# Performance work log

Hardware: AMD Instinct MI355X
Metric: run time of the kernel (lower is better)

## Reference

```python
import jax, jax.numpy as jnp
import numpy as np

OBS_DIM = 4096
NUM_ACTIONS = 18
ACTION_DIM = 64
D_MODEL = 512
N_LAYERS = 4
HIST = 256
BATCH = 32
D_STATE = 16
D_CONV = 4
EXPAND = 2
D_INNER = EXPAND * D_MODEL           # 1024
DT_RANK = -(-D_MODEL // 16)          # ceil(512/16)=32
OBS_OUT = D_MODEL - ACTION_DIM       # 448


def setup_inputs() -> dict:
    key = jax.random.key(0)
    ks = jax.random.split(key, 16)
    s = 0.02
    inp = {
        "obss": jax.random.normal(ks[0], (BATCH, HIST, OBS_DIM), jnp.float32),
        "actions": jax.random.randint(ks[1], (BATCH, HIST, 1), 0, NUM_ACTIONS),
        "obs_W": jax.random.normal(ks[2], (OBS_OUT, OBS_DIM), jnp.float32) * s,
        "obs_b": jnp.zeros((OBS_OUT,), jnp.float32),
        "act_emb": jax.random.normal(ks[3], (NUM_ACTIONS, ACTION_DIM), jnp.float32) * s,
        "pos_emb": jax.random.normal(ks[4], (1, HIST, D_MODEL), jnp.float32) * s,
        # stacked Mamba params, leading dim = N_LAYERS
        "W_in": jax.random.normal(ks[5], (N_LAYERS, 2 * D_INNER, D_MODEL), jnp.float32) * s,
        "conv_w": jax.random.normal(ks[6], (N_LAYERS, D_INNER, D_CONV), jnp.float32) * s,
        "conv_b": jnp.zeros((N_LAYERS, D_INNER), jnp.float32),
        "W_x": jax.random.normal(ks[7], (N_LAYERS, DT_RANK + 2 * D_STATE, D_INNER), jnp.float32) * s,
        "W_dt": jax.random.normal(ks[8], (N_LAYERS, D_INNER, DT_RANK), jnp.float32) * s,
        "b_dt": jnp.full((N_LAYERS, D_INNER), -4.6, jnp.float32),  # softplus(-4.6)~0.01
        "A_log": jnp.log(jnp.broadcast_to(jnp.arange(1, D_STATE + 1, dtype=jnp.float32), (N_LAYERS, D_INNER, D_STATE))),
        "D_p": jnp.ones((N_LAYERS, D_INNER), jnp.float32),
        "W_out": jax.random.normal(ks[9], (N_LAYERS, D_MODEL, D_INNER), jnp.float32) * s,
        "ffn_W1": jax.random.normal(ks[10], (D_MODEL, D_MODEL), jnp.float32) * s,
        "ffn_b1": jnp.zeros((D_MODEL,), jnp.float32),
        "ffn_W2": jax.random.normal(ks[11], (NUM_ACTIONS, D_MODEL), jnp.float32) * s,
        "ffn_b2": jnp.zeros((NUM_ACTIONS,), jnp.float32),
    }
    return inp


def mamba_block(x, W_in, conv_w, conv_b, W_x, W_dt, b_dt, A_log, D_p, W_out):
    # x: (B, L, D_MODEL)
    B_, L, _ = x.shape
    xz = jnp.einsum('bld,ed->ble', x, W_in)            # (B,L,2*Di)
    xi, z = jnp.split(xz, 2, axis=-1)
    # causal depthwise conv1d, kernel D_CONV
    xp = jnp.pad(xi, ((0, 0), (D_CONV - 1, 0), (0, 0)))
    xc = conv_b + sum(conv_w[:, k] * xp[:, k:k + L, :] for k in range(D_CONV))
    xc = jax.nn.silu(xc)                               # (B,L,Di)
    xdbl = jnp.einsum('bld,ed->ble', xc, W_x)          # (B,L,dt_rank+2*ds)
    dt, Bm, Cm = jnp.split(xdbl, [DT_RANK, DT_RANK + D_STATE], axis=-1)
    dt = jax.nn.softplus(jnp.einsum('blr,dr->bld', dt, W_dt) + b_dt)  # (B,L,Di)
    A = -jnp.exp(A_log)                                # (Di,ds)

    def step(h, inp):
        dt_t, B_t, C_t, x_t = inp                      # (B,Di),(B,ds),(B,ds),(B,Di)
        dA = jnp.exp(dt_t[:, :, None] * A)             # (B,Di,ds)
        h = dA * h + dt_t[:, :, None] * B_t[:, None, :] * x_t[:, :, None]
        y = jnp.einsum('bdn,bn->bd', h, C_t)
        return h, y

    h0 = jnp.zeros((B_, D_INNER, D_STATE), xc.dtype)
    xs = (dt.transpose(1, 0, 2), Bm.transpose(1, 0, 2),
          Cm.transpose(1, 0, 2), xc.transpose(1, 0, 2))
    _, ys = jax.lax.scan(step, h0, xs)                 # (L,B,Di)
    y = ys.transpose(1, 0, 2) + xc * D_p
    y = y * jax.nn.silu(z)
    return jnp.einsum('bld,ed->ble', y, W_out)         # (B,L,D_MODEL)


def reference(obss, actions, obs_W, obs_b, act_emb, pos_emb, W_in, conv_w, conv_b,
              W_x, W_dt, b_dt, A_log, D_p, W_out, ffn_W1, ffn_b1, ffn_W2, ffn_b2):
    L = obss.shape[1]
    tok = jnp.einsum('blo,eo->ble', obss, obs_W) + obs_b          # (B,L,448)
    ae = act_emb[actions[:, :, 0]]                                # (B,L,64)
    # torch.roll(ae, 1, 1) with first step zeroed (history_len > 1)
    ae = jnp.concatenate([jnp.zeros_like(ae[:, :1]), ae[:, :-1]], axis=1)
    x = jnp.concatenate([ae, tok], axis=-1) + pos_emb[:, :L, :]   # (B,L,512)
    for i in range(N_LAYERS):
        x = mamba_block(x, W_in[i], conv_w[i], conv_b[i], W_x[i], W_dt[i],
                        b_dt[i], A_log[i], D_p[i], W_out[i])
    h = jax.nn.relu(jnp.einsum('bld,ed->ble', x, ffn_W1) + ffn_b1)
    out = jnp.einsum('bld,ed->ble', h, ffn_W2) + ffn_b2           # (B,L,18)
    return out[:, -L:, :]
```

## Files before the change

kernel.cpp:

```cpp
#include <hip/hip_runtime.h>
#include <hip/hip_bf16.h>
#include <cstdint>
#include <cstddef>

#define HIST    256
#define DMODEL  512
#define DINNER  1024
#define DSTATE  16
#define DTRANK  32
#define OBSDIM  4096
#define OBSOUT  448
#define ADIM    64
#define NLAYERS 4
#define MROWS   8192

typedef __bf16  bf16x8 __attribute__((ext_vector_type(8)));
typedef float   f32x4  __attribute__((ext_vector_type(4)));

enum { MEPI_TOK = 0, MEPI_BF16 = 1, MEPI_SPLIT = 2, MEPI_RELUB = 3 };

__device__ __forceinline__ float siluf(float x) { return x / (1.f + __expf(-x)); }
__device__ __forceinline__ float softplusf(float x) {
    return fmaxf(x, 0.f) + log1pf(__expf(-fabsf(x)));
}
__device__ __forceinline__ float bflo(unsigned u) { return __uint_as_float(u << 16); }
__device__ __forceinline__ float bfhi(unsigned u) { return __uint_as_float(u & 0xffff0000u); }

template<int EPI>
__global__ __launch_bounds__(256)
void gemm_mfma(const __hip_bfloat16* __restrict__ A, int lda,
               const __hip_bfloat16* __restrict__ W,
               float* __restrict__ Cf, int ldc,
               __hip_bfloat16* __restrict__ Cb, int ldcb,
               int coff, int N, int K, int nbn,
               const float* __restrict__ bias, const float* __restrict__ pos)
{
    __shared__ __hip_bfloat16 Asm[2][128 * 32];
    __shared__ __hip_bfloat16 Bsm[2][128 * 32];
    const int bid = blockIdx.x;
    const int xcd = bid & 7;
    const int s   = bid >> 3;
    const int n_blk = s % nbn;
    const int m_blk = xcd * ((int)(gridDim.x >> 3) / nbn) + s / nbn;
    const int m0 = m_blk * 128;
    const int n0 = n_blk * 128;

    const int tid  = threadIdx.x;
    const int lane = tid & 63;
    const int wv   = tid >> 6;
    const int wm   = (wv >> 1) << 6;
    const int wn   = (wv & 1) << 6;
    const int sr   = lane >> 2;
    const int sc   = (lane & 3) << 3;
    const int quad = lane >> 4;
    const int c16  = lane & 15;

    f32x4 acc[4][4] = {};
    const __hip_bfloat16* aptr = A + (size_t)(m0 + wv * 16 + sr) * lda + sc;
    const __hip_bfloat16* bptr = W + (size_t)(n0 + wv * 16 + sr) * K + sc;

#define STAGE(K0, BUF) { \
    __hip_bfloat16* asml = Asm[BUF] + wv * 16 * 32; \
    __hip_bfloat16* bsml = Bsm[BUF] + wv * 16 * 32; \
    __builtin_amdgcn_global_load_lds( \
        (const __attribute__((address_space(1))) void*)(aptr + (K0)), \
        (__attribute__((address_space(3))) void*)(asml), 16, 0, 0); \
    __builtin_amdgcn_global_load_lds( \
        (const __attribute__((address_space(1))) void*)(aptr + (size_t)64 * lda + (K0)), \
        (__attribute__((address_space(3))) void*)(asml + 64 * 32), 16, 0, 0); \
    __builtin_amdgcn_global_load_lds( \
        (const __attribute__((address_space(1))) void*)(bptr + (K0)), \
        (__attribute__((address_space(3))) void*)(bsml), 16, 0, 0); \
    __builtin_amdgcn_global_load_lds( \
        (const __attribute__((address_space(1))) void*)(bptr + (size_t)64 * K + (K0)), \
        (__attribute__((address_space(3))) void*)(bsml + 64 * 32), 16, 0, 0); \
    }

    STAGE(0, 0)
    __syncthreads();
    int cur = 0;
    for (int k0 = 0; k0 < K; k0 += 32) {
        if (k0 + 32 < K) STAGE(k0 + 32, cur ^ 1)

        bf16x8 af[4], bfr[4];
        #pragma unroll
        for (int i = 0; i < 4; ++i) {
            af[i]  = *(const bf16x8*)(Asm[cur] + (wm + i * 16 + c16) * 32 + quad * 8);
            bfr[i] = *(const bf16x8*)(Bsm[cur] + (wn + i * 16 + c16) * 32 + quad * 8);
        }
        #pragma unroll
        for (int i = 0; i < 4; ++i)
            #pragma unroll
            for (int j = 0; j < 4; ++j)
                acc[i][j] = __builtin_amdgcn_mfma_f32_16x16x32_bf16(af[i], bfr[j], acc[i][j], 0, 0, 0);

        __syncthreads();
        cur ^= 1;
    }
#undef STAGE

    #pragma unroll
    for (int i = 0; i < 4; ++i) {
        const int mbase = m0 + wm + i * 16 + quad * 4;
        #pragma unroll
        for (int j = 0; j < 4; ++j) {
            const int n = n0 + wn + j * 16 + c16;
            if (n < N) {
                #pragma unroll
                for (int r = 0; r < 4; ++r) {
                    const size_t m = mbase + r;
                    float v = acc[i][j][r];
                    if (EPI == MEPI_TOK) {
                        v += bias[n] + pos[(m & (HIST - 1)) * DMODEL + coff + n];
                        Cb[m * ldcb + coff + n] = __float2bfloat16(v);
                    } else if (EPI == MEPI_BF16) {
                        Cb[m * ldcb + n] = __float2bfloat16(v);
                    } else if (EPI == MEPI_SPLIT) {
                        if (n < DTRANK) Cf[m * 32 + n] = v;
                        else Cb[(m >> 1) * 64 + (n & 15) * 4 + (m & 1) * 2 + ((n >> 4) & 1)]
                                 = __float2bfloat16(v);
                    } else {
                        Cb[m * ldcb + n] = __float2bfloat16(fmaxf(v + bias[n], 0.f));
                    }
                }
            }
        }
    }
}

__global__ __launch_bounds__(256)
void gemm_f32_sp(const float* __restrict__ A, int lda,
                 const float* __restrict__ W,
                 __hip_bfloat16* __restrict__ C, int ldc,
                 int N, int K, const float* __restrict__ bias)
{
    __shared__ float As[32][68];
    __shared__ float Ws[32][68];
    const int tid = threadIdx.x;
    const int tx = tid & 15, ty = tid >> 4;
    const int m0 = blockIdx.y * 64;
    const int n0 = blockIdx.x * 64;
    const int lr = tid >> 3;
    const int lc = (tid & 7) << 2;
    float acc[4][4] = {};
    for (int k0 = 0; k0 < K; k0 += 32) {
        const float4 a0 = *(const float4*)(A + (size_t)(m0 + lr) * lda + k0 + lc);
        const float4 a1 = *(const float4*)(A + (size_t)(m0 + lr + 32) * lda + k0 + lc);
        const float4 b0 = *(const float4*)(W + (size_t)(n0 + lr) * K + k0 + lc);
        const float4 b1 = *(const float4*)(W + (size_t)(n0 + lr + 32) * K + k0 + lc);
        __syncthreads();
        As[lc+0][lr] = a0.x; As[lc+1][lr] = a0.y; As[lc+2][lr] = a0.z; As[lc+3][lr] = a0.w;
        As[lc+0][lr+32] = a1.x; As[lc+1][lr+32] = a1.y; As[lc+2][lr+32] = a1.z; As[lc+3][lr+32] = a1.w;
        Ws[lc+0][lr] = b0.x; Ws[lc+1][lr] = b0.y; Ws[lc+2][lr] = b0.z; Ws[lc+3][lr] = b0.w;
        Ws[lc+0][lr+32] = b1.x; Ws[lc+1][lr+32] = b1.y; Ws[lc+2][lr+32] = b1.z; Ws[lc+3][lr+32] = b1.w;
        __syncthreads();
        #pragma unroll
        for (int k = 0; k < 32; ++k) {
            const float4 a4 = *(const float4*)&As[k][ty << 2];
            const float4 b4 = *(const float4*)&Ws[k][tx << 2];
            const float a[4] = {a4.x, a4.y, a4.z, a4.w};
            const float b[4] = {b4.x, b4.y, b4.z, b4.w};
            #pragma unroll
            for (int i = 0; i < 4; ++i)
                #pragma unroll
                for (int j = 0; j < 4; ++j)
                    acc[i][j] = fmaf(a[i], b[j], acc[i][j]);
        }
    }
    const int mb = m0 + (ty << 2);
    const int nb = n0 + (tx << 2);
    #pragma unroll
    for (int i = 0; i < 4; ++i) {
        const size_t m = mb + i;
        #pragma unroll
        for (int j = 0; j < 4; ++j) {
            const int n = nb + j;
            C[m * ldc + n] = __float2bfloat16(softplusf(acc[i][j] + bias[n]));
        }
    }
}

__global__ __launch_bounds__(256)
void cast_bf16_kernel(const float* __restrict__ src, __hip_bfloat16* __restrict__ dst, int n4)
{
    const int i = blockIdx.x * 256 + threadIdx.x;
    if (i >= n4) return;
    const float4 v = ((const float4*)src)[i];
    union { __hip_bfloat16 h[4]; short4 s; } o;
    o.h[0] = __float2bfloat16(v.x); o.h[1] = __float2bfloat16(v.y);
    o.h[2] = __float2bfloat16(v.z); o.h[3] = __float2bfloat16(v.w);
    ((short4*)dst)[i] = o.s;
}

__global__ __launch_bounds__(256)
void cast_pad_kernel(const float* __restrict__ src, __hip_bfloat16* __restrict__ dst,
                     int nrows, int K4, int total4)
{
    const int i = blockIdx.x * 256 + threadIdx.x;
    if (i >= total4) return;
    const int row = i / K4;
    float4 v = make_float4(0.f, 0.f, 0.f, 0.f);
    if (row < nrows) v = ((const float4*)src)[i];
    union { __hip_bfloat16 h[4]; short4 s; } o;
    o.h[0] = __float2bfloat16(v.x); o.h[1] = __float2bfloat16(v.y);
    o.h[2] = __float2bfloat16(v.z); o.h[3] = __float2bfloat16(v.w);
    ((short4*)dst)[i] = o.s;
}

__global__ __launch_bounds__(256)
void embed_kernel(const int* __restrict__ actions, const float* __restrict__ act_emb,
                  const float* __restrict__ pos_emb, __hip_bfloat16* __restrict__ xb)
{
    const int idx = blockIdx.x * 256 + threadIdx.x;
    const int e = idx & 63;
    const int m = idx >> 6;
    const int l = m & (HIST - 1);
    const int b = m >> 8;
    float v = pos_emb[l * DMODEL + e];
    if (l > 0) {
        const int a = actions[b * HIST + l - 1];
        v += act_emb[a * ADIM + e];
    }
    xb[(size_t)m * DMODEL + e] = __float2bfloat16(v);
}

__global__ __launch_bounds__(256)
void conv_silu_kernel(const __hip_bfloat16* __restrict__ xzb, const float* __restrict__ cw,
                      const float* __restrict__ cb, __hip_bfloat16* __restrict__ xcb)
{
    const int idx = blockIdx.x * 256 + threadIdx.x;
    const int d = idx & (DINNER - 1);
    const int m = idx >> 10;
    const int l = m & (HIST - 1);
    const float4 w = ((const float4*)cw)[d];
    const __hip_bfloat16* basep = xzb + (size_t)m * (2 * DINNER) + d;
    float acc = cb[d] + w.w * __bfloat162float(basep[0]);
    if (l >= 1) acc = fmaf(w.z, __bfloat162float(basep[-2 * DINNER]), acc);
    if (l >= 2) acc = fmaf(w.y, __bfloat162float(basep[-4 * DINNER]), acc);
    if (l >= 3) acc = fmaf(w.x, __bfloat162float(basep[-6 * DINNER]), acc);
    xcb[idx] = __float2bfloat16(siluf(acc));
}

__device__ __forceinline__ float dpp_add(float x, const int ctrl) {
    switch (ctrl) {
    case 0xB1:  return x + __int_as_float(__builtin_amdgcn_update_dpp(0, __float_as_int(x), 0xB1, 0xF, 0xF, true));
    case 0x4E:  return x + __int_as_float(__builtin_amdgcn_update_dpp(0, __float_as_int(x), 0x4E, 0xF, 0xF, true));
    case 0x141: return x + __int_as_float(__builtin_amdgcn_update_dpp(0, __float_as_int(x), 0x141, 0xF, 0xF, true));
    default:    return x + __int_as_float(__builtin_amdgcn_update_dpp(0, __float_as_int(x), 0x140, 0xF, 0xF, true));
    }
}

__global__ __launch_bounds__(256)
void scan_kernel(const __hip_bfloat16* __restrict__ dtb, const __hip_bfloat16* __restrict__ bcb,
                 const __hip_bfloat16* __restrict__ xcb, const __hip_bfloat16* __restrict__ zb,
                 const float* __restrict__ A_log, const float* __restrict__ D_p,
                 __hip_bfloat16* __restrict__ yb)
{
    __shared__ unsigned sdx2[128][32];
    __shared__ unsigned sbc2[128][32];
    __shared__ unsigned short sz[256][16];
    const int tid = threadIdx.x;
    const int n   = tid & 15;
    const int g   = tid >> 4;
    const int c0  = blockIdx.x * 16;
    const int b   = c0 >> 10;
    const int d0  = c0 & (DINNER - 1);
    const int d   = d0 + g;
    const size_t row0 = (size_t)b * HIST;

    {
        const uint4* src = (const uint4*)((const unsigned short*)bcb + row0 * 32);
        uint4* dst = (uint4*)&sbc2[0][0];
        #pragma unroll
        for (int i = 0; i < 4; ++i) dst[tid + i * 256] = src[tid + i * 256];
    }
    {
        const int P = tid >> 1, half = tid & 1;
        const size_t m0r = row0 + 2 * P, m1r = m0r + 1;
        const unsigned short* dtu = (const unsigned short*)dtb;
        const unsigned short* xcu = (const unsigned short*)xcb;
        union { uint4 u; unsigned short s[8]; } D0, D1, X0, X1;
        D0.u = *(const uint4*)(dtu + m0r * DINNER + d0 + half * 8);
        D1.u = *(const uint4*)(dtu + m1r * DINNER + d0 + half * 8);
        X0.u = *(const uint4*)(xcu + m0r * DINNER + d0 + half * 8);
        X1.u = *(const uint4*)(xcu + m1r * DINNER + d0 + half * 8);
        #pragma unroll
        for (int gp = 0; gp < 8; ++gp) {
            sdx2[P][(half * 8 + gp) * 2]     = (unsigned)D0.s[gp] | ((unsigned)X0.s[gp] << 16);
            sdx2[P][(half * 8 + gp) * 2 + 1] = (unsigned)D1.s[gp] | ((unsigned)X1.s[gp] << 16);
        }
    }
    {
        const int l = tid >> 1, half = tid & 1;
        const unsigned short* zu = (const unsigned short*)zb;
        #pragma unroll
        for (int i = 0; i < 2; ++i) {
            const int ll = l + i * 128;
            *(uint4*)&sz[ll][half * 8] =
                *(const uint4*)(zu + (row0 + ll) * 2 * DINNER + d0 + half * 8);
        }
    }
    __syncthreads();

    const float A  = -__expf(A_log[d * DSTATE + n]);
    const float Dp = D_p[d];
    float h = 0.f;

    for (int l0 = 0; l0 < HIST; l0 += 16) {
        float yreg = 0.f;
        #pragma unroll
        for (int jp = 0; jp < 8; ++jp) {
            const int P = (l0 >> 1) + jp;
            const uint2 q  = *(const uint2*)&sdx2[P][g * 2];
            const uint2 r2 = *(const uint2*)&sbc2[P][n * 2];
            {
                const float dt = bflo(q.x), xc = bfhi(q.x);
                const float Bv = bflo(r2.x), Cv = bfhi(r2.x);
                const float dA = __expf(dt * A);
                h = fmaf(dA, h, dt * xc * Bv);
                float ctr = h * Cv;
                ctr = dpp_add(ctr, 0xB1);
                ctr = dpp_add(ctr, 0x4E);
                ctr = dpp_add(ctr, 0x141);
                ctr = dpp_add(ctr, 0x140);
                if (n == 2 * jp) yreg = ctr;
            }
            {
                const float dt = bflo(q.y), xc = bfhi(q.y);
                const float Bv = bflo(r2.y), Cv = bfhi(r2.y);
                const float dA = __expf(dt * A);
                h = fmaf(dA, h, dt * xc * Bv);
                float ctr = h * Cv;
                ctr = dpp_add(ctr, 0xB1);
                ctr = dpp_add(ctr, 0x4E);
                ctr = dpp_add(ctr, 0x141);
                ctr = dpp_add(ctr, 0x140);
                if (n == 2 * jp + 1) yreg = ctr;
            }
        }
        const int lr = l0 + n;
        const unsigned short xcu16 =
            ((const unsigned short*)sdx2)[(lr >> 1) * 64 + g * 4 + 1 + 2 * (lr & 1)];
        const float xcf = __uint_as_float(((unsigned)xcu16) << 16);
        const float ze = __uint_as_float(((unsigned)sz[lr][g]) << 16);
        yb[(row0 + lr) * DINNER + d] =
            __float2bfloat16((yreg + xcf * Dp) * siluf(ze));
    }
}

__global__ __launch_bounds__(256)
void ffn2_kernel(const __hip_bfloat16* __restrict__ h, const float* __restrict__ W2,
                 const float* __restrict__ b2, float* __restrict__ out)
{
    const int idx = blockIdx.x * 256 + threadIdx.x;
    const int n = idx & 31;
    const int m = idx >> 5;
    if (n >= 18) return;
    const unsigned short* hr = (const unsigned short*)(h + (size_t)m * DMODEL);
    const float* wr = W2 + (size_t)n * DMODEL;
    float acc = b2[n];
    for (int k = 0; k < DMODEL; k += 8) {
        const uint4 hv = *(const uint4*)(hr + k);
        const float4 w0 = *(const float4*)(wr + k);
        const float4 w1 = *(const float4*)(wr + k + 4);
        acc = fmaf(bflo(hv.x), w0.x, acc);
        acc = fmaf(bfhi(hv.x), w0.y, acc);
        acc = fmaf(bflo(hv.y), w0.z, acc);
        acc = fmaf(bfhi(hv.y), w0.w, acc);
        acc = fmaf(bflo(hv.z), w1.x, acc);
        acc = fmaf(bfhi(hv.z), w1.y, acc);
        acc = fmaf(bflo(hv.w), w1.z, acc);
        acc = fmaf(bfhi(hv.w), w1.w, acc);
    }
    out[(size_t)m * 18 + n] = acc;
}

extern "C" void kernel_launch(void* const* d_in, const int* in_sizes, int n_in,
                              void* d_out, int out_size, void* d_ws, size_t ws_size,
                              hipStream_t stream)
{
    const float* obss    = (const float*)d_in[0];
    const int*   actions = (const int*)  d_in[1];
    const float* obs_W   = (const float*)d_in[2];
    const float* obs_b   = (const float*)d_in[3];
    const float* act_emb = (const float*)d_in[4];
    const float* pos_emb = (const float*)d_in[5];
    const float* W_in    = (const float*)d_in[6];
    const float* conv_w  = (const float*)d_in[7];
    const float* conv_b  = (const float*)d_in[8];
    const float* W_x     = (const float*)d_in[9];
    const float* W_dt    = (const float*)d_in[10];
    const float* b_dt    = (const float*)d_in[11];
    const float* A_log   = (const float*)d_in[12];
    const float* D_p     = (const float*)d_in[13];
    const float* W_out   = (const float*)d_in[14];
    const float* ffn_W1  = (const float*)d_in[15];
    const float* ffn_b1  = (const float*)d_in[16];
    const float* ffn_W2  = (const float*)d_in[17];
    const float* ffn_b2  = (const float*)d_in[18];
    float* out = (float*)d_out;

    const size_t MiB = 1024 * 1024;
    char* base = (char*)d_ws;
    __hip_bfloat16* xb    = (__hip_bfloat16*)(base);
    __hip_bfloat16* xzb   = (__hip_bfloat16*)(base + 8 * MiB);
    __hip_bfloat16* xcb   = (__hip_bfloat16*)(base + 40 * MiB);
    __hip_bfloat16* dtb   = (__hip_bfloat16*)(base + 56 * MiB);
    __hip_bfloat16* yb    = (__hip_bfloat16*)(base + 88 * MiB);
    float*          xdt   = (float*)(base + 104 * MiB);
    __hip_bfloat16* bcb   = (__hip_bfloat16*)(base + 105 * MiB);
    __hip_bfloat16* wbuf  = (__hip_bfloat16*)(base + 106 * MiB);
    __hip_bfloat16* wxb   = (__hip_bfloat16*)(base + 110 * MiB);
    __hip_bfloat16* obssb = (__hip_bfloat16*)(base + 8 * MiB);
    __hip_bfloat16* hbuf  = (__hip_bfloat16*)(base + 8 * MiB);

    cast_bf16_kernel<<<(MROWS * OBSDIM / 4) / 256, 256, 0, stream>>>(obss, obssb, MROWS * OBSDIM / 4);
    cast_pad_kernel<<<(512 * OBSDIM / 4) / 256, 256, 0, stream>>>(obs_W, wbuf, OBSOUT, OBSDIM / 4, 512 * OBSDIM / 4);
    embed_kernel<<<MROWS * ADIM / 256, 256, 0, stream>>>(actions, act_emb, pos_emb, xb);
    gemm_mfma<MEPI_TOK><<<4 * (MROWS / 128), 256, 0, stream>>>(
        obssb, OBSDIM, wbuf, nullptr, 0, xb, DMODEL, ADIM, OBSOUT, OBSDIM, 4, obs_b, pos_emb);

    for (int i = 0; i < NLAYERS; ++i) {
        cast_bf16_kernel<<<(2 * DINNER * DMODEL / 4) / 256, 256, 0, stream>>>(
            W_in + (size_t)i * 2 * DINNER * DMODEL, wbuf, 2 * DINNER * DMODEL / 4);
        gemm_mfma<MEPI_BF16><<<(2 * DINNER / 128) * (MROWS / 128), 256, 0, stream>>>(
            xb, DMODEL, wbuf, nullptr, 0, xzb, 2 * DINNER, 0, 2 * DINNER, DMODEL,
            2 * DINNER / 128, nullptr, nullptr);
        conv_silu_kernel<<<MROWS * DINNER / 256, 256, 0, stream>>>(
            xzb, conv_w + (size_t)i * DINNER * 4, conv_b + (size_t)i * DINNER, xcb);
        cast_pad_kernel<<<(128 * DINNER / 4) / 256, 256, 0, stream>>>(
            W_x + (size_t)i * 64 * DINNER, wxb, 64, DINNER / 4, 128 * DINNER / 4);
        gemm_mfma<MEPI_SPLIT><<<MROWS / 128, 256, 0, stream>>>(
            xcb, DINNER, wxb, xdt, 0, bcb, 0, 0, 64, DINNER, 1, nullptr, nullptr);
        gemm_f32_sp<<<dim3(DINNER / 64, MROWS / 64), 256, 0, stream>>>(
            xdt, 32, W_dt + (size_t)i * DINNER * DTRANK, dtb, DINNER, DINNER, DTRANK,
            b_dt + (size_t)i * DINNER);
        scan_kernel<<<(32 * DINNER) / 16, 256, 0, stream>>>(
            dtb, bcb, xcb, xzb + DINNER, A_log + (size_t)i * DINNER * DSTATE,
            D_p + (size_t)i * DINNER, yb);
        cast_bf16_kernel<<<(DMODEL * DINNER / 4) / 256, 256, 0, stream>>>(
            W_out + (size_t)i * DMODEL * DINNER, wbuf, DMODEL * DINNER / 4);
        gemm_mfma<MEPI_BF16><<<(DMODEL / 128) * (MROWS / 128), 256, 0, stream>>>(
            yb, DINNER, wbuf, nullptr, 0, xb, DMODEL, 0, DMODEL, DINNER,
            DMODEL / 128, nullptr, nullptr);
    }

    cast_bf16_kernel<<<(DMODEL * DMODEL / 4) / 256, 256, 0, stream>>>(ffn_W1, wbuf, DMODEL * DMODEL / 4);
    gemm_mfma<MEPI_RELUB><<<(DMODEL / 128) * (MROWS / 128), 256, 0, stream>>>(
        xb, DMODEL, wbuf, nullptr, 0, hbuf, DMODEL, 0, DMODEL, DMODEL,
        DMODEL / 128, ffn_b1, nullptr);
    ffn2_kernel<<<MROWS * 32 / 256, 256, 0, stream>>>(hbuf, ffn_W2, ffn_b2, out);
}
```

Before: 1.283 ms.

## Double-buffer selective-scan inputs in chunks and overlap loads with recurrence

The scan kernel no longer stages the whole 256-step sequence into shared memory before computing. It now loads 64-step chunks into double-buffered, padded, transposed LDS tiles, prefetching the next chunk into registers while the current one is processed. It also remaps block indices so neighbouring blocks interleave across batches, uses exp2 with a prescaled A, and reads z straight into registers. The intent is to hide global load latency behind the serial recurrence and to cut LDS footprint so more blocks fit per CU, at the cost of more barriers and extra register pressure.

```diff
diff --git a/kernel.cpp b/kernel.cpp
--- a/kernel.cpp
+++ b/kernel.cpp
@@ -256,96 +256,116 @@
                  const float* __restrict__ A_log, const float* __restrict__ D_p,
                  __hip_bfloat16* __restrict__ yb)
 {
-    __shared__ unsigned sdx2[128][32];
-    __shared__ unsigned sbc2[128][32];
-    __shared__ unsigned short sz[256][16];
+    __shared__ unsigned sdx[2][16][68];
+    __shared__ unsigned sbc[2][16][68];
+
     const int tid = threadIdx.x;
     const int n   = tid & 15;
     const int g   = tid >> 4;
-    const int c0  = blockIdx.x * 16;
+
+    const int bid = blockIdx.x;
+    const int blk = ((bid & 7) << 8) | (bid >> 3);
+    const int c0  = blk * 16;
     const int b   = c0 >> 10;
     const int d0  = c0 & (DINNER - 1);
     const int d   = d0 + g;
     const size_t row0 = (size_t)b * HIST;
 
-    {
-        const uint4* src = (const uint4*)((const unsigned short*)bcb + row0 * 32);
-        uint4* dst = (uint4*)&sbc2[0][0];
-        #pragma unroll
-        for (int i = 0; i < 4; ++i) dst[tid + i * 256] = src[tid + i * 256];
-    }
-    {
-        const int P = tid >> 1, half = tid & 1;
-        const size_t m0r = row0 + 2 * P, m1r = m0r + 1;
-        const unsigned short* dtu = (const unsigned short*)dtb;
-        const unsigned short* xcu = (const unsigned short*)xcb;
-        union { uint4 u; unsigned short s[8]; } D0, D1, X0, X1;
-        D0.u = *(const uint4*)(dtu + m0r * DINNER + d0 + half * 8);
-        D1.u = *(const uint4*)(dtu + m1r * DINNER + d0 + half * 8);
-        X0.u = *(const uint4*)(xcu + m0r * DINNER + d0 + half * 8);
-        X1.u = *(const uint4*)(xcu + m1r * DINNER + d0 + half * 8);
-        #pragma unroll
-        for (int gp = 0; gp < 8; ++gp) {
-            sdx2[P][(half * 8 + gp) * 2]     = (unsigned)D0.s[gp] | ((unsigned)X0.s[gp] << 16);
-            sdx2[P][(half * 8 + gp) * 2 + 1] = (unsigned)D1.s[gp] | ((unsigned)X1.s[gp] << 16);
-        }
-    }
-    {
-        const int l = tid >> 1, half = tid & 1;
-        const unsigned short* zu = (const unsigned short*)zb;
-        #pragma unroll
-        for (int i = 0; i < 2; ++i) {
-            const int ll = l + i * 128;
-            *(uint4*)&sz[ll][half * 8] =
-                *(const uint4*)(zu + (row0 + ll) * 2 * DINNER + d0 + half * 8);
-        }
-    }
-    __syncthreads();
-
-    const float A  = -__expf(A_log[d * DSTATE + n]);
+    const int sr = tid >> 2;
+    const int sq = tid & 3;
+    const unsigned short* dtu = (const unsigned short*)dtb;
+    const unsigned short* xcu = (const unsigned short*)xcb;
+    const unsigned short* zu  = (const unsigned short*)zb;
+    const unsigned*       bcu = (const unsigned*)bcb;
+
+    const float Ar = -__expf(A_log[d * DSTATE + n]);
+#if __has_builtin(__builtin_amdgcn_exp2f)
+    const float A2 = Ar * 1.44269504089f;
+#define DAEXP(x) __builtin_amdgcn_exp2f((x) * A2)
+#else
+#define DAEXP(x) __expf((x) * Ar)
+#endif
     const float Dp = D_p[d];
     float h = 0.f;
 
-    for (int l0 = 0; l0 < HIST; l0 += 16) {
-        float yreg = 0.f;
-        #pragma unroll
-        for (int jp = 0; jp < 8; ++jp) {
-            const int P = (l0 >> 1) + jp;
-            const uint2 q  = *(const uint2*)&sdx2[P][g * 2];
-            const uint2 r2 = *(const uint2*)&sbc2[P][n * 2];
-            {
-                const float dt = bflo(q.x), xc = bfhi(q.x);
-                const float Bv = bflo(r2.x), Cv = bfhi(r2.x);
-                const float dA = __expf(dt * A);
-                h = fmaf(dA, h, dt * xc * Bv);
-                float ctr = h * Cv;
-                ctr = dpp_add(ctr, 0xB1);
-                ctr = dpp_add(ctr, 0x4E);
-                ctr = dpp_add(ctr, 0x141);
-                ctr = dpp_add(ctr, 0x140);
-                if (n == 2 * jp) yreg = ctr;
+    uint2 dv, xv; uint4 bv;
+    unsigned short za[4], znx[4];
+
+#define SLOAD(cc) { \
+    const size_t rb = (row0 + (size_t)(cc) * 64 + sr) * DINNER + d0 + sq * 4; \
+    dv = *(const uint2*)(dtu + rb); \
+    xv = *(const uint2*)(xcu + rb); \
+    bv = *(const uint4*)(bcu + row0 * 16 + (size_t)(cc) * 1024 + tid * 4); \
+}
+#define SWRITE(bb) { \
+    const int ch = sq * 4; \
+    sdx[bb][ch + 0][sr] = (dv.x & 0xffffu) | (xv.x << 16); \
+    sdx[bb][ch + 1][sr] = (dv.x >> 16)     | (xv.x & 0xffff0000u); \
+    sdx[bb][ch + 2][sr] = (dv.y & 0xffffu) | (xv.y << 16); \
+    sdx[bb][ch + 3][sr] = (dv.y >> 16)     | (xv.y & 0xffff0000u); \
+    const int e2 = (tid & 7) * 2, p2 = (tid >> 3) * 2; \
+    sbc[bb][e2 + 0][p2 + 0] = bv.x; \
+    sbc[bb][e2 + 0][p2 + 1] = bv.y; \
+    sbc[bb][e2 + 1][p2 + 0] = bv.z; \
+    sbc[bb][e2 + 1][p2 + 1] = bv.w; \
+}
+#define ZLOAD(cc, arr) { \
+    _Pragma("unroll") \
+    for (int w = 0; w < 4; ++w) \
+        arr[w] = zu[(row0 + (size_t)(cc) * 64 + w * 16 + n) * (2 * DINNER) + d0 + g]; \
+}
+#define SSTEP(Q, R, KK) { \
+    const float dt = bflo(Q), xc = bfhi(Q); \
+    const float Bv = bflo(R), Cv = bfhi(R); \
+    const float dA = DAEXP(dt); \
+    h = fmaf(dA, h, dt * xc * Bv); \
+    float ctr = h * Cv; \
+    ctr = dpp_add(ctr, 0xB1); \
+    ctr = dpp_add(ctr, 0x4E); \
+    ctr = dpp_add(ctr, 0x141); \
+    ctr = dpp_add(ctr, 0x140); \
+    if (n == (KK)) yreg = ctr; \
+}
+
+    SLOAD(0)
+    ZLOAD(0, za)
+    SWRITE(0)
+    __syncthreads();
+
+    for (int c = 0; c < 4; ++c) {
+        const int buf = c & 1;
+        if (c < 3) { SLOAD(c + 1) ZLOAD(c + 1, znx) }
+
+        const unsigned (*sdxc)[68] = sdx[buf];
+        const unsigned (*sbcc)[68] = sbc[buf];
+        #pragma unroll
+        for (int w = 0; w < 4; ++w) {
+            float yreg = 0.f;
+            #pragma unroll
+            for (int jq = 0; jq < 4; ++jq) {
+                const uint4 qv = *(const uint4*)&sdxc[g][w * 16 + jq * 4];
+                const uint4 rv = *(const uint4*)&sbcc[n][w * 16 + jq * 4];
+                SSTEP(qv.x, rv.x, jq * 4 + 0)
+                SSTEP(qv.y, rv.y, jq * 4 + 1)
+                SSTEP(qv.z, rv.z, jq * 4 + 2)
+                SSTEP(qv.w, rv.w, jq * 4 + 3)
             }
-            {
-                const float dt = bflo(q.y), xc = bfhi(q.y);
-                const float Bv = bflo(r2.y), Cv = bfhi(r2.y);
-                const float dA = __expf(dt * A);
-                h = fmaf(dA, h, dt * xc * Bv);
-                float ctr = h * Cv;
-                ctr = dpp_add(ctr, 0xB1);
-                ctr = dpp_add(ctr, 0x4E);
-                ctr = dpp_add(ctr, 0x141);
-                ctr = dpp_add(ctr, 0x140);
-                if (n == 2 * jp + 1) yreg = ctr;
-            }
+            const float xcf = bfhi(sdxc[g][w * 16 + n]);
+            const float ze  = __uint_as_float((unsigned)za[w] << 16);
+            yb[(row0 + c * 64 + w * 16 + n) * DINNER + d] =
+                __float2bfloat16((yreg + xcf * Dp) * siluf(ze));
         }
-        const int lr = l0 + n;
-        const unsigned short xcu16 =
-            ((const unsigned short*)sdx2)[(lr >> 1) * 64 + g * 4 + 1 + 2 * (lr & 1)];
-        const float xcf = __uint_as_float(((unsigned)xcu16) << 16);
-        const float ze = __uint_as_float(((unsigned)sz[lr][g]) << 16);
-        yb[(row0 + lr) * DINNER + d] =
-            __float2bfloat16((yreg + xcf * Dp) * siluf(ze));
-    }
+
+        if (c < 3) SWRITE((c + 1) & 1)
+        __syncthreads();
+        #pragma unroll
+        for (int w = 0; w < 4; ++w) za[w] = znx[w];
+    }
+#undef SLOAD
+#undef SWRITE
+#undef ZLOAD
+#undef SSTEP
+#undef DAEXP
 }
 
 __global__ __launch_bounds__(256)
```

Measured after the change: 1.220 ms. 4.9% less time.
